# Kernel tuning notes

Hardware: AMD Instinct MI355X
Metric: run time of the kernel (lower is better)

## Reference

```python
import jax, jax.numpy as jnp
import numpy as np

NEIGHBOR_K = 3

def setup_inputs() -> dict:
    key = jax.random.key(0)
    k1, k2 = jax.random.split(key)
    query_fea = jax.random.normal(k1, (8, 75, 121, 640), dtype=jnp.float32)
    support_fea = jax.random.normal(k2, (8, 5, 5, 121, 640), dtype=jnp.float32)
    return {"query_fea": query_fea, "support_fea": support_fea}

def reference(query_fea, support_fea):
    # query_fea: [b, n_wq, patch_num, dim]
    # support_fea: [b, way, shot, patch_num, dim]
    b, way, shot, pn, dim = support_fea.shape
    sup = support_fea.reshape(b, way, shot * pn, dim)  # [b, way, S, dim]
    # inner products between every query patch and every support patch
    # sim: [b, n_wq, way, patch_num, S]
    sim = jnp.einsum('bqpd,bwsd->bqwps', query_fea, sup)
    # top-k over support patches (last axis), then mean over all topk values
    topk = jax.lax.top_k(sim, NEIGHBOR_K)[0]  # [b, n_wq, way, patch_num, k]
    return jnp.mean(topk, axis=(-2, -1))  # [b, n_wq, way]
```

## Files before the change

kernel.cpp:

```cpp
#include <hip/hip_runtime.h>
#include <hip/hip_bf16.h>

#define BATCH 8
#define NQ    75
#define WAY   5
#define PN    121
#define DIM   640
#define SSZ   605
#define TOPK  3

#define KCH 10
#define NCH 5

#define NQTILES 6000
#define NSTILES 2000
#define WS_NEED   ((size_t)(NQTILES + NSTILES) * 16384)

typedef __attribute__((ext_vector_type(8))) short   short8;
typedef __attribute__((ext_vector_type(8))) __bf16  bf16x8;
typedef __attribute__((ext_vector_type(4))) float   f32x4;

__device__ inline unsigned short f2bf(float f) {
  unsigned u = __builtin_bit_cast(unsigned, f);
  return (unsigned short)((u + 0x7fffu + ((u >> 16) & 1u)) >> 16);
}
__device__ inline unsigned pk2(float lo, float hi) {
  return (unsigned)f2bf(lo) | ((unsigned)f2bf(hi) << 16);
}

__device__ inline void ins3(float &a, float &b, float &c, float v) {
  float na  = fmaxf(a, v);
  float nb  = __builtin_amdgcn_fmed3f(v, a, b);
  float nc2 = __builtin_amdgcn_fmed3f(v, b, c);
  a = na; b = nb; c = nc2;
}

__device__ inline void async_copy16(const void* g, void* l) {
  __builtin_amdgcn_global_load_lds(
      (const __attribute__((address_space(1))) unsigned int*)g,
      (__attribute__((address_space(3))) unsigned int*)l, 16, 0, 0);
}

__device__ __forceinline__ void pack_unit(int unit_b, int j,
                                          const float* __restrict__ qf,
                                          const float* __restrict__ sf,
                                          uint4* __restrict__ wq,
                                          uint4* __restrict__ wsp) {
  const float* src;
  uint4* dstbase;
  int nrows, rowbase;
  if (j < 300) {
    const int q = j >> 2;
    rowbase = (j & 3) << 5;
    const int slab = unit_b * NQ + q;
    src = qf + (size_t)slab * PN * DIM;
    dstbase = wq + (size_t)slab * KCH * 1024;
    nrows = PN;
  } else {
    const int l = j - 300;
    rowbase = (l & 3) << 5;
    const int fi = l >> 2;
    const int nc = fi % NCH;
    const int w  = fi / NCH;
    const int bw = unit_b * WAY + w;
    const int uv = bw * NCH + nc;
    src = sf + ((size_t)bw * SSZ + nc * 128) * DIM;
    dstbase = wsp + (size_t)uv * KCH * 1024;
    nrows = SSZ - nc * 128; if (nrows > 128) nrows = 128;
  }
  #pragma unroll 2
  for (int i = 0; i < 10; ++i) {
    const int L    = i * 256 + threadIdx.x;
    const int rowl = L / 80;
    const int s    = L - rowl * 80;
    const int row  = rowbase + rowl;
    const int kc   = s >> 3;
    const int c    = s & 7;
    const int p    = c ^ (row & 7);
    uint4 o = make_uint4(0u, 0u, 0u, 0u);
    if (row < nrows) {
      const float* g = src + (size_t)row * DIM + s * 8;
      float4 v0 = reinterpret_cast<const float4*>(g)[0];
      float4 v1 = reinterpret_cast<const float4*>(g)[1];
      o.x = pk2(v0.x, v0.y); o.y = pk2(v0.z, v0.w);
      o.z = pk2(v1.x, v1.y); o.w = pk2(v1.z, v1.w);
    }
    dstbase[(size_t)kc * 1024 + row * 8 + p] = o;
  }
}

__global__ __launch_bounds__(256) void cvt_pack(const float* __restrict__ qf,
                                                const float* __restrict__ sf,
                                                uint4* __restrict__ wq,
                                                uint4* __restrict__ wsp) {
  const int blk = blockIdx.x;
  int b, j0;
  if (blk < 1200) { const int slab = blk >> 1; b = slab / NQ;
    j0 = (slab - b * NQ) * 4 + (blk & 1) * 2; }
  else { const int u = blk - 1200; const int uv = u >> 1;
    const int bw = uv / NCH; b = bw / WAY;
    const int fi = (bw - b * WAY) * NCH + (uv % NCH);
    j0 = 300 + fi * 4 + (u & 1) * 2; }
  pack_unit(b, j0, qf, sf, wq, wsp);
  pack_unit(b, j0 + 1, qf, sf, wq, wsp);
}

__global__ __launch_bounds__(512, 2) void lpc_main(
    const char* __restrict__ wq,
    const char* __restrict__ wsp,
    float* __restrict__ out)
{
  __shared__ char As[2][32768];
  __shared__ char Bs[2][16384];
  __shared__ float red[8];

  const int sbid = blockIdx.x;
  const int b    = sbid & 7;
  const int bid2 = sbid >> 3;
  const int w    = bid2 % WAY;
  const int qp   = bid2 / WAY;
  const int q0   = qp * 2;

  const char* Qt0 = wq + (size_t)(b * NQ + q0) * KCH * 16384;
  const char* Qt1 = Qt0 + (size_t)KCH * 16384;
  const char* St  = wsp + (size_t)(b * WAY + w) * NCH * KCH * 16384;

  const int tid  = threadIdx.x;
  const int lane = tid & 63;
  const int wv   = tid >> 6;
  const int l15  = lane & 15;
  const int quad = lane >> 4;
  const int mrow0 = (wv >> 1) * 64;
  const int ncol0 = (wv & 1) * 64;

  const int sw16 = (l15 & 7) * 16;
  const int cp0  = (quad * 16) ^ sw16;
  const int cp1  = ((4 + quad) * 16) ^ sw16;

  auto stage = [&](int buf, int tt, int kcc) {
    const char* a0 = Qt0 + (size_t)kcc * 16384;
    const char* a1 = Qt1 + (size_t)kcc * 16384;
    const char* bb = St  + (size_t)tt  * 16384;
    #pragma unroll
    for (int i = 0; i < 6; ++i) {
      const int c = wv * 6 + i;
      const char* src = (c < 16) ? a0 + c * 1024
                      : (c < 32) ? a1 + (c - 16) * 1024
                                 : bb + (c - 32) * 1024;
      char* dst = (c < 32) ? &As[buf][0] + c * 1024
                           : &Bs[buf][0] + (c - 32) * 1024;
      async_copy16(src + lane * 16, dst);
    }
  };

  float t3a[4][4], t3b[4][4], t3c[4][4];
  #pragma unroll
  for (int mt = 0; mt < 4; ++mt)
    #pragma unroll
    for (int r = 0; r < 4; ++r) {
      t3a[mt][r] = -3.0e38f; t3b[mt][r] = -3.0e38f; t3c[mt][r] = -3.0e38f;
    }

  stage(0, 0, 0);
  __syncthreads();

  f32x4 acc[4][4];
  int cur = 0, kc = 0, nc = 0;

  #pragma unroll 1
  for (int t = 0; t < NCH * KCH; ++t) {
    if (kc == 0) {
      #pragma unroll
      for (int mt = 0; mt < 4; ++mt)
        #pragma unroll
        for (int nt = 0; nt < 4; ++nt)
          acc[mt][nt] = (f32x4){0.f, 0.f, 0.f, 0.f};
    }

    if (t < NCH * KCH - 1) {
      const int kc2 = (kc == 9) ? 0 : kc + 1;
      stage(cur ^ 1, t + 1, kc2);
    }

    const char* qb = &As[cur][0] + (mrow0 + l15) * 128;
    const char* sb = &Bs[cur][0] + (ncol0 + l15) * 128;
    #pragma unroll
    for (int kk = 0; kk < 2; ++kk) {
      const int cp = kk ? cp1 : cp0;
      short8 a[4], bf[4];
      #pragma unroll
      for (int mt = 0; mt < 4; ++mt)
        a[mt] = *reinterpret_cast<const short8*>(qb + mt * 2048 + cp);
      #pragma unroll
      for (int nt = 0; nt < 4; ++nt)
        bf[nt] = *reinterpret_cast<const short8*>(sb + nt * 2048 + cp);
      #pragma unroll
      for (int mt = 0; mt < 4; ++mt)
        #pragma unroll
        for (int nt = 0; nt < 4; ++nt)
          acc[mt][nt] = __builtin_amdgcn_mfma_f32_16x16x32_bf16(
              __builtin_bit_cast(bf16x8, a[mt]),
              __builtin_bit_cast(bf16x8, bf[nt]), acc[mt][nt], 0, 0, 0);
    }

    if (kc == 9) {
      #pragma unroll
      for (int nt = 0; nt < 4; ++nt) {
        const int col = nc * 128 + ncol0 + nt * 16 + l15;
        const bool valid = col < SSZ;
        #pragma unroll
        for (int mt = 0; mt < 4; ++mt)
          #pragma unroll
          for (int r = 0; r < 4; ++r) {
            float v = valid ? acc[mt][nt][r] : -3.0e38f;
            ins3(t3a[mt][r], t3b[mt][r], t3c[mt][r], v);
          }
      }
      kc = 0; ++nc;
    } else {
      ++kc;
    }

    __syncthreads();
    cur ^= 1;
  }

  #pragma unroll
  for (int m = 1; m < 16; m <<= 1) {
    #pragma unroll
    for (int mt = 0; mt < 4; ++mt)
      #pragma unroll
      for (int r = 0; r < 4; ++r) {
        float o0 = __shfl_xor(t3a[mt][r], m);
        float o1 = __shfl_xor(t3b[mt][r], m);
        float o2 = __shfl_xor(t3c[mt][r], m);
        ins3(t3a[mt][r], t3b[mt][r], t3c[mt][r], o0);
        ins3(t3a[mt][r], t3b[mt][r], t3c[mt][r], o1);
        ins3(t3a[mt][r], t3b[mt][r], t3c[mt][r], o2);
      }
  }

  float* tb = reinterpret_cast<float*>(As);
  __syncthreads();
  if ((wv & 1) == 1 && l15 == 0) {
    #pragma unroll
    for (int mt = 0; mt < 4; ++mt)
      #pragma unroll
      for (int r = 0; r < 4; ++r) {
        int row = mrow0 + mt * 16 + quad * 4 + r;
        tb[row * 3 + 0] = t3a[mt][r];
        tb[row * 3 + 1] = t3b[mt][r];
        tb[row * 3 + 2] = t3c[mt][r];
      }
  }
  __syncthreads();
  if ((wv & 1) == 0 && l15 == 0) {
    #pragma unroll
    for (int mt = 0; mt < 4; ++mt)
      #pragma unroll
      for (int r = 0; r < 4; ++r) {
        int row = mrow0 + mt * 16 + quad * 4 + r;
        ins3(t3a[mt][r], t3b[mt][r], t3c[mt][r], tb[row * 3 + 0]);
        ins3(t3a[mt][r], t3b[mt][r], t3c[mt][r], tb[row * 3 + 1]);
        ins3(t3a[mt][r], t3b[mt][r], t3c[mt][r], tb[row * 3 + 2]);
      }
  }
  __syncthreads();
  if ((wv & 1) == 0 && l15 == 0) {
    #pragma unroll
    for (int mt = 0; mt < 4; ++mt)
      #pragma unroll
      for (int r = 0; r < 4; ++r) {
        int row = mrow0 + mt * 16 + quad * 4 + r;
        tb[row * 3 + 0] = t3a[mt][r];
        tb[row * 3 + 1] = t3b[mt][r];
        tb[row * 3 + 2] = t3c[mt][r];
      }
  }
  __syncthreads();

  const int half = tid >> 8;
  float s = 0.f;
  for (int j = tid & 255; j < PN * TOPK; j += 256) s += tb[half * 384 + j];
  #pragma unroll
  for (int off = 32; off > 0; off >>= 1) s += __shfl_down(s, off);
  if (lane == 0) red[wv] = s;
  __syncthreads();
  if (tid == 0)
    out[(size_t)(b * NQ + q0) * WAY + w] =
        (red[0] + red[1] + red[2] + red[3]) * (1.0f / (PN * TOPK));
  if (tid == 256 && q0 + 1 < NQ)
    out[(size_t)(b * NQ + q0 + 1) * WAY + w] =
        (red[4] + red[5] + red[6] + red[7]) * (1.0f / (PN * TOPK));
}

__global__ __launch_bounds__(256) void lpc_fallback(
    const float* __restrict__ qf, const float* __restrict__ sf,
    float* __restrict__ out)
{
  __shared__ short Qst[128][72];
  __shared__ short Sst[64][72];
  __shared__ float Cs[128][67];
  __shared__ float top3[128][TOPK];
  __shared__ float red[4];

  const int bid = blockIdx.x;
  const int w   = bid % WAY;
  const int qi  = (bid / WAY) % NQ;
  const int b   = bid / (WAY * NQ);
  const float* Qb = qf + ((size_t)(b * NQ + qi)) * PN * DIM;
  const float* Sb = sf + ((size_t)(b * WAY + w)) * SSZ * DIM;
  const int tid  = threadIdx.x;
  const int lane = tid & 63;
  const int wv   = tid >> 6;
  const int l15  = lane & 15;
  const int quad = lane >> 4;

  if (tid < 128) { top3[tid][0] = -3.0e38f; top3[tid][1] = -3.0e38f; top3[tid][2] = -3.0e38f; }
  f32x4 acc[2][4];
  for (int nc = 0; nc < 10; ++nc) {
    const int sbase = nc * 64;
    int vn = SSZ - sbase; if (vn > 64) vn = 64;
    #pragma unroll
    for (int mt = 0; mt < 2; ++mt)
      #pragma unroll
      for (int nt = 0; nt < 4; ++nt) acc[mt][nt] = (f32x4){0.f,0.f,0.f,0.f};
    for (int kc = 0; kc < KCH; ++kc) {
      const int kbase = kc * 64;
      __syncthreads();
      #pragma unroll
      for (int i = 0; i < 8; ++i) {
        int lin = i * 256 + tid; int row = lin >> 4; int c4 = lin & 15;
        float4 v = make_float4(0.f,0.f,0.f,0.f);
        if (row < PN) v = *reinterpret_cast<const float4*>(Qb + (size_t)row * DIM + kbase + c4 * 4);
        ushort4 h; h.x=f2bf(v.x); h.y=f2bf(v.y); h.z=f2bf(v.z); h.w=f2bf(v.w);
        *reinterpret_cast<ushort4*>(&Qst[row][c4*4]) = h;
      }
      #pragma unroll
      for (int i = 0; i < 4; ++i) {
        int lin = i * 256 + tid; int row = lin >> 4; int c4 = lin & 15;
        int srow = sbase + row;
        float4 v = make_float4(0.f,0.f,0.f,0.f);
        if (srow < SSZ) v = *reinterpret_cast<const float4*>(Sb + (size_t)srow * DIM + kbase + c4 * 4);
        ushort4 h; h.x=f2bf(v.x); h.y=f2bf(v.y); h.z=f2bf(v.z); h.w=f2bf(v.w);
        *reinterpret_cast<ushort4*>(&Sst[row][c4*4]) = h;
      }
      __syncthreads();
      #pragma unroll
      for (int kk = 0; kk < 2; ++kk) {
        bf16x8 a0 = __builtin_bit_cast(bf16x8, *reinterpret_cast<const short8*>(&Qst[wv*32+ 0+l15][kk*32+quad*8]));
        bf16x8 a1 = __builtin_bit_cast(bf16x8, *reinterpret_cast<const short8*>(&Qst[wv*32+16+l15][kk*32+quad*8]));
        #pragma unroll
        for (int nt = 0; nt < 4; ++nt) {
          bf16x8 bb = __builtin_bit_cast(bf16x8, *reinterpret_cast<const short8*>(&Sst[nt*16+l15][kk*32+quad*8]));
          acc[0][nt] = __builtin_amdgcn_mfma_f32_16x16x32_bf16(a0, bb, acc[0][nt], 0,0,0);
          acc[1][nt] = __builtin_amdgcn_mfma_f32_16x16x32_bf16(a1, bb, acc[1][nt], 0,0,0);
        }
      }
    }
    #pragma unroll
    for (int mt = 0; mt < 2; ++mt)
      #pragma unroll
      for (int nt = 0; nt < 4; ++nt)
        #pragma unroll
        for (int r = 0; r < 4; ++r)
          Cs[wv*32+mt*16+quad*4+r][nt*16+l15] = acc[mt][nt][r];
    __syncthreads();
    {
      int row = tid >> 1; int half = tid & 1;
      float a = -3.0e38f, b2 = -3.0e38f, c = -3.0e38f;
      int c0 = half * 32; int cend = c0 + 32; if (cend > vn) cend = vn;
      for (int cc = c0; cc < cend; ++cc) ins3(a, b2, c, Cs[row][cc]);
      float o0 = __shfl_xor(a,1), o1 = __shfl_xor(b2,1), o2 = __shfl_xor(c,1);
      ins3(a,b2,c,o0); ins3(a,b2,c,o1); ins3(a,b2,c,o2);
      if (half == 0) {
        float r0=top3[row][0], r1=top3[row][1], r2=top3[row][2];
        ins3(r0,r1,r2,a); ins3(r0,r1,r2,b2); ins3(r0,r1,r2,c);
        top3[row][0]=r0; top3[row][1]=r1; top3[row][2]=r2;
      }
    }
    __syncthreads();
  }
  float s = 0.f;
  for (int i = tid; i < PN * TOPK; i += 256) s += top3[i/TOPK][i%TOPK];
  #pragma unroll
  for (int off = 32; off > 0; off >>= 1) s += __shfl_down(s, off);
  if (lane == 0) red[wv] = s;
  __syncthreads();
  if (tid == 0) out[bid] = (red[0]+red[1]+red[2]+red[3]) * (1.0f/(PN*TOPK));
}

extern "C" void kernel_launch(void* const* d_in, const int* in_sizes, int n_in,
                              void* d_out, int out_size, void* d_ws, size_t ws_size,
                              hipStream_t stream) {
  const float* qf = (const float*)d_in[0];
  const float* sf = (const float*)d_in[1];
  float* out = (float*)d_out;
  (void)in_sizes; (void)n_in; (void)out_size;

  if (ws_size >= WS_NEED && d_ws != nullptr) {
    uint4* wq  = (uint4*)d_ws;
    uint4* wsp = wq + (size_t)NQTILES * 1024;
    cvt_pack<<<1600, 256, 0, stream>>>(qf, sf, wq, wsp);
    lpc_main<<<BATCH * NQ * WAY / 2 + BATCH * WAY / 2, 512, 0, stream>>>(
        (const char*)wq, (const char*)wsp, out);
  } else {
    lpc_fallback<<<BATCH * NQ * WAY, 256, 0, stream>>>(qf, sf, out);
  }
}
```

Measured before the change: 711.8 us.

## Process three queries per block with 12 waves and split-wave async staging

Each block now handles three query slabs instead of two with 768 threads, so each staged support tile is reused across more query rows, lowering global traffic per FLOP. Loading is split so waves 0-7 fetch query tiles and waves 8-11 fetch support tiles. Staging is issued two steps ahead with explicit vmcnt waits and raw s_barrier instead of __syncthreads, and MFMA sections get raised wave priority. The larger LDS footprint (about 128KB) and 768-thread blocks reduce how many blocks fit per CU, and the hand-written waitcnt accounting is fragile.

```diff
diff --git a/kernel.cpp b/kernel.cpp
--- a/kernel.cpp
+++ b/kernel.cpp
@@ -105,24 +105,23 @@
   pack_unit(b, j0 + 1, qf, sf, wq, wsp);
 }
 
-__global__ __launch_bounds__(512, 2) void lpc_main(
+__global__ __launch_bounds__(768, 3) void lpc_main(
     const char* __restrict__ wq,
     const char* __restrict__ wsp,
     float* __restrict__ out)
 {
-  __shared__ char As[2][32768];
+  __shared__ char As[2][49152];
   __shared__ char Bs[2][16384];
-  __shared__ float red[8];
+  __shared__ float red[12];
 
   const int sbid = blockIdx.x;
   const int b    = sbid & 7;
   const int bid2 = sbid >> 3;
   const int w    = bid2 % WAY;
-  const int qp   = bid2 / WAY;
-  const int q0   = qp * 2;
+  const int qt   = bid2 / WAY;
+  const int q0   = qt * 3;
 
   const char* Qt0 = wq + (size_t)(b * NQ + q0) * KCH * 16384;
-  const char* Qt1 = Qt0 + (size_t)KCH * 16384;
   const char* St  = wsp + (size_t)(b * WAY + w) * NCH * KCH * 16384;
 
   const int tid  = threadIdx.x;
@@ -138,18 +137,21 @@
   const int cp1  = ((4 + quad) * 16) ^ sw16;
 
   auto stage = [&](int buf, int tt, int kcc) {
-    const char* a0 = Qt0 + (size_t)kcc * 16384;
-    const char* a1 = Qt1 + (size_t)kcc * 16384;
-    const char* bb = St  + (size_t)tt  * 16384;
-    #pragma unroll
-    for (int i = 0; i < 6; ++i) {
-      const int c = wv * 6 + i;
-      const char* src = (c < 16) ? a0 + c * 1024
-                      : (c < 32) ? a1 + (c - 16) * 1024
-                                 : bb + (c - 32) * 1024;
-      char* dst = (c < 32) ? &As[buf][0] + c * 1024
-                           : &Bs[buf][0] + (c - 32) * 1024;
-      async_copy16(src + lane * 16, dst);
+    if (wv < 8) {
+      #pragma unroll
+      for (int i = 0; i < 6; ++i) {
+        const int ch = wv * 6 + i;
+        const char* src = Qt0 + (size_t)(ch >> 4) * (KCH * 16384)
+                        + (size_t)kcc * 16384 + (ch & 15) * 1024;
+        async_copy16(src + lane * 16, &As[buf][0] + ch * 1024);
+      }
+    } else {
+      #pragma unroll
+      for (int i = 0; i < 4; ++i) {
+        const int ch = (wv - 8) * 4 + i;
+        const char* src = St + (size_t)tt * 16384 + ch * 1024;
+        async_copy16(src + lane * 16, &Bs[buf][0] + ch * 1024);
+      }
     }
   };
 
@@ -162,13 +164,15 @@
     }
 
   stage(0, 0, 0);
-  __syncthreads();
+  stage(1, 1, 1);
 
   f32x4 acc[4][4];
-  int cur = 0, kc = 0, nc = 0;
+  int kc = 0, nc = 0, kc2 = 2;
 
   #pragma unroll 1
   for (int t = 0; t < NCH * KCH; ++t) {
+    const int cur = t & 1;
+
     if (kc == 0) {
       #pragma unroll
       for (int mt = 0; mt < 4; ++mt)
@@ -177,13 +181,18 @@
           acc[mt][nt] = (f32x4){0.f, 0.f, 0.f, 0.f};
     }
 
-    if (t < NCH * KCH - 1) {
-      const int kc2 = (kc == 9) ? 0 : kc + 1;
-      stage(cur ^ 1, t + 1, kc2);
-    }
+    if (t < 49) {
+      if (wv < 8) asm volatile("s_waitcnt vmcnt(6)" ::: "memory");
+      else        asm volatile("s_waitcnt vmcnt(4)" ::: "memory");
+    } else {
+      asm volatile("s_waitcnt vmcnt(0)" ::: "memory");
+    }
+    asm volatile("s_barrier" ::: "memory");
 
     const char* qb = &As[cur][0] + (mrow0 + l15) * 128;
     const char* sb = &Bs[cur][0] + (ncol0 + l15) * 128;
+
+    __builtin_amdgcn_s_setprio(1);
     #pragma unroll
     for (int kk = 0; kk < 2; ++kk) {
       const int cp = kk ? cp1 : cp0;
@@ -202,6 +211,7 @@
               __builtin_bit_cast(bf16x8, a[mt]),
               __builtin_bit_cast(bf16x8, bf[nt]), acc[mt][nt], 0, 0, 0);
     }
+    __builtin_amdgcn_s_setprio(0);
 
     if (kc == 9) {
       #pragma unroll
@@ -221,8 +231,10 @@
       ++kc;
     }
 
-    __syncthreads();
-    cur ^= 1;
+    asm volatile("s_barrier" ::: "memory");
+
+    if (t < 48) stage(cur, t + 2, kc2);
+    kc2 = (kc2 == 9) ? 0 : kc2 + 1;
   }
 
   #pragma unroll
@@ -240,7 +252,7 @@
       }
   }
 
-  float* tb = reinterpret_cast<float*>(As);
+  float* tb = reinterpret_cast<float*>(&As[0][0]);
   __syncthreads();
   if ((wv & 1) == 1 && l15 == 0) {
     #pragma unroll
@@ -279,19 +291,19 @@
   }
   __syncthreads();
 
-  const int half = tid >> 8;
+  const int third = tid >> 8;
   float s = 0.f;
-  for (int j = tid & 255; j < PN * TOPK; j += 256) s += tb[half * 384 + j];
+  for (int j = tid & 255; j < PN * TOPK; j += 256) s += tb[third * 384 + j];
   #pragma unroll
   for (int off = 32; off > 0; off >>= 1) s += __shfl_down(s, off);
   if (lane == 0) red[wv] = s;
   __syncthreads();
-  if (tid == 0)
-    out[(size_t)(b * NQ + q0) * WAY + w] =
-        (red[0] + red[1] + red[2] + red[3]) * (1.0f / (PN * TOPK));
-  if (tid == 256 && q0 + 1 < NQ)
-    out[(size_t)(b * NQ + q0 + 1) * WAY + w] =
-        (red[4] + red[5] + red[6] + red[7]) * (1.0f / (PN * TOPK));
+  if ((tid & 255) == 0) {
+    const int r0 = third * 4;
+    out[(size_t)(b * NQ + q0 + third) * WAY + w] =
+        (red[r0] + red[r0 + 1] + red[r0 + 2] + red[r0 + 3]) *
+        (1.0f / (PN * TOPK));
+  }
 }
 
 __global__ __launch_bounds__(256) void lpc_fallback(
@@ -402,8 +414,7 @@
     uint4* wq  = (uint4*)d_ws;
     uint4* wsp = wq + (size_t)NQTILES * 1024;
     cvt_pack<<<1600, 256, 0, stream>>>(qf, sf, wq, wsp);
-    lpc_main<<<BATCH * NQ * WAY / 2 + BATCH * WAY / 2, 512, 0, stream>>>(
-        (const char*)wq, (const char*)wsp, out);
+    lpc_main<<<1000, 768, 0, stream>>>((const char*)wq, (const char*)wsp, out);
   } else {
     lpc_fallback<<<BATCH * NQ * WAY, 256, 0, stream>>>(qf, sf, out);
   }
```

Measured after the change: 1.094 ms. 1.54x slower.
